# Kernel optimization log

Hardware: AMD Instinct MI355X
Metric: run time of the kernel (lower is better)

The kernel has to match this reference:

```python
import jax, jax.numpy as jnp
import numpy as np

B, N, H = 131072, 64, 8  # batch, n_agents (= n states = n coupling pins, ring), hidden width


def setup_inputs() -> dict:
    key = jax.random.key(0)
    ks = jax.random.split(key, 9)
    x = jax.random.normal(ks[0], (B, N), jnp.float32)
    # per-agent intrinsic MLP (heterogeneous agents, vectorized over agent dim)
    W1 = jax.random.normal(ks[1], (N, H), jnp.float32) * 0.5
    b1 = jax.random.normal(ks[2], (N, H), jnp.float32) * 0.1
    W2 = jax.random.normal(ks[3], (N, H), jnp.float32) * 0.5
    b2 = jax.random.normal(ks[4], (N,), jnp.float32) * 0.1
    # shared coupling MLP: takes [x_send, x_recv] -> scalar contribution
    Wc1 = jax.random.normal(ks[5], (2, H), jnp.float32) * 0.5
    bc1 = jax.random.normal(ks[6], (H,), jnp.float32) * 0.1
    Wc2 = jax.random.normal(ks[7], (H,), jnp.float32) * 0.5
    bc2 = jax.random.normal(ks[8], (1,), jnp.float32) * 0.1
    send_idx = jnp.arange(N, dtype=jnp.int32)
    recv_idx = (send_idx + 1) % N  # ring topology pins (send -> receive), symmetric coupling
    return dict(x=x, W1=W1, b1=b1, W2=W2, b2=b2, Wc1=Wc1, bc1=bc1,
                Wc2=Wc2, bc2=bc2, send_idx=send_idx, recv_idx=recv_idx)


def reference(x, W1, b1, W2, b2, Wc1, bc1, Wc2, bc2, send_idx, recv_idx):
    # ---- coupling_physics: gather pin features, shared MLP, symmetric scatter-add ----
    feats = jnp.stack([x[:, send_idx], x[:, recv_idx]], axis=-1)        # [B, E, 2]
    hc = jnp.tanh(jnp.einsum('bef,fh->beh', feats, Wc1) + bc1)          # [B, E, H]
    contrib = jnp.einsum('beh,h->be', hc, Wc2) + bc2                    # [B, E]
    interactions = (jnp.zeros_like(x)
                    .at[:, recv_idx].add(contrib)    # dx[:, receive] += contribution
                    .at[:, send_idx].add(-contrib))  # dx[:, send]    -= contribution (symmetric)
    # ---- intrinsic_physics: per-agent MLP on own state, plus aggregated interactions ----
    ha = jnp.tanh(x[..., None] * W1 + b1)                               # [B, N, H]
    dx = jnp.einsum('bnh,nh->bn', ha, W2) + b2 + interactions           # [B, N]
    return dx  # [:, :outsize] with outsize == N
```

## Files before the change

kernel.cpp:

```cpp
#include <hip/hip_runtime.h>

static constexpr int N_AGENTS = 64;
static constexpr int H_DIM    = 8;

__device__ __forceinline__ float fast_exp2(float v) {
#if __has_builtin(__builtin_amdgcn_exp2f)
    return __builtin_amdgcn_exp2f(v);
#else
    return exp2f(v);
#endif
}

__device__ __forceinline__ float fast_rcp(float v) {
#if __has_builtin(__builtin_amdgcn_rcpf)
    return __builtin_amdgcn_rcpf(v);
#else
    return 1.0f / v;
#endif
}

__device__ __forceinline__ float fast_tanh(float v) {
    float z = fast_exp2(v * 2.8853900817779268f);
    float r = fast_rcp(z + 1.0f);
    return __builtin_fmaf(-2.0f, r, 1.0f);
}

__global__ __launch_bounds__(256) void networked_ode_kernel(
    const float* __restrict__ x,
    const float* __restrict__ W1,
    const float* __restrict__ b1,
    const float* __restrict__ W2,
    const float* __restrict__ b2,
    const float* __restrict__ Wc1,
    const float* __restrict__ bc1,
    const float* __restrict__ Wc2,
    const float* __restrict__ bc2,
    const int* __restrict__ send_idx,
    const int* __restrict__ recv_idx,
    float* __restrict__ out,
    int B)
{
    const int lane           = threadIdx.x & 63;
    const int wave_in_block  = threadIdx.x >> 6;
    const int waves_per_blk  = blockDim.x >> 6;
    const int gwave          = blockIdx.x * waves_per_blk + wave_in_block;
    const int total_waves    = gridDim.x * waves_per_blk;

    float w1[H_DIM], bb1[H_DIM], w2[H_DIM];
#pragma unroll
    for (int h = 0; h < H_DIM; ++h) {
        w1[h]  = W1[lane * H_DIM + h];
        bb1[h] = b1[lane * H_DIM + h];
        w2[h]  = W2[lane * H_DIM + h];
    }
    const float b2v = b2[lane];

    float wcs[H_DIM], wcr[H_DIM], bc1v[H_DIM], wc2v[H_DIM];
#pragma unroll
    for (int h = 0; h < H_DIM; ++h) {
        wcs[h]  = Wc1[h];
        wcr[h]  = Wc1[H_DIM + h];
        bc1v[h] = bc1[h];
        wc2v[h] = Wc2[h];
    }
    const float bc2v = bc2[0];

    const int sidx = send_idx[lane];
    const int ridx = recv_idx[lane];

    __shared__ int inv_r_s[256], inv_s_s[256];
    const int base = wave_in_block * 64;
    inv_r_s[base + ridx] = lane;
    inv_s_s[base + sidx] = lane;
    __syncthreads();
    const int inv_r = inv_r_s[base + lane];
    const int inv_s = inv_s_s[base + lane];

    for (int row = gwave; row < B; row += total_waves) {
        const float xv = x[(size_t)row * N_AGENTS + lane];
        const float xs = __shfl(xv, sidx, 64);
        const float xr = __shfl(xv, ridx, 64);

        float c = bc2v;
#pragma unroll
        for (int h = 0; h < H_DIM; ++h) {
            float a = __builtin_fmaf(xs, wcs[h], __builtin_fmaf(xr, wcr[h], bc1v[h]));
            c = __builtin_fmaf(fast_tanh(a), wc2v[h], c);
        }

        float acc = b2v;
#pragma unroll
        for (int h = 0; h < H_DIM; ++h) {
            float a = __builtin_fmaf(xv, w1[h], bb1[h]);
            acc = __builtin_fmaf(fast_tanh(a), w2[h], acc);
        }

        const float cr = __shfl(c, inv_r, 64);
        const float cs = __shfl(c, inv_s, 64);

        out[(size_t)row * N_AGENTS + lane] = acc + cr - cs;
    }
}

extern "C" void kernel_launch(void* const* d_in, const int* in_sizes, int n_in,
                              void* d_out, int out_size, void* d_ws, size_t ws_size,
                              hipStream_t stream) {
    const float* x   = (const float*)d_in[0];
    const float* W1  = (const float*)d_in[1];
    const float* b1  = (const float*)d_in[2];
    const float* W2  = (const float*)d_in[3];
    const float* b2  = (const float*)d_in[4];
    const float* Wc1 = (const float*)d_in[5];
    const float* bc1 = (const float*)d_in[6];
    const float* Wc2 = (const float*)d_in[7];
    const float* bc2 = (const float*)d_in[8];
    const int* send_idx = (const int*)d_in[9];
    const int* recv_idx = (const int*)d_in[10];

    const int B = in_sizes[0] / N_AGENTS;

    const int blocks = 2048;
    networked_ode_kernel<<<blocks, dim3(256), 0, stream>>>(
        x, W1, b1, W2, b2, Wc1, bc1, Wc2, bc2, send_idx, recv_idx,
        (float*)d_out, B);
}
```

Before: 130.5 us.

## Use packed fp16 rational tanh and process four rows per wave iteration

Replaces the fp32 exp2/rcp tanh with a clamped Padé rational approximation evaluated in packed half2 arithmetic, where the reciprocal is a bit-trick seed refined by two Newton steps. Each wave now handles four rows per iteration, pairing rows into half2 lanes. It also skips the send shuffle when the send index is the identity. The aim is to cut transcendental and ALU cost per element. In exchange, accumulation and output are done in fp16, which loses precision and may exceed the tolerance.

```diff
diff --git a/kernel.cpp b/kernel.cpp
--- a/kernel.cpp
+++ b/kernel.cpp
@@ -1,28 +1,47 @@
 #include <hip/hip_runtime.h>
+
+typedef _Float16 h2 __attribute__((ext_vector_type(2)));
+typedef unsigned short u2 __attribute__((ext_vector_type(2)));
 
 static constexpr int N_AGENTS = 64;
 static constexpr int H_DIM    = 8;
+static constexpr int ROWS     = 4;
 
-__device__ __forceinline__ float fast_exp2(float v) {
-#if __has_builtin(__builtin_amdgcn_exp2f)
-    return __builtin_amdgcn_exp2f(v);
+__device__ __forceinline__ h2 h2splat(float v) {
+    _Float16 h = (_Float16)v;
+    return (h2){h, h};
+}
+
+__device__ __forceinline__ h2 pack2(float a, float b) {
+#if __has_builtin(__builtin_amdgcn_cvt_pkrtz)
+    auto r = __builtin_amdgcn_cvt_pkrtz(a, b);
+    h2 out; __builtin_memcpy(&out, &r, 4); return out;
 #else
-    return exp2f(v);
+    return (h2){(_Float16)a, (_Float16)b};
 #endif
 }
 
-__device__ __forceinline__ float fast_rcp(float v) {
-#if __has_builtin(__builtin_amdgcn_rcpf)
-    return __builtin_amdgcn_rcpf(v);
-#else
-    return 1.0f / v;
-#endif
-}
+struct TanhConsts {
+    h2 c3p5, mc3p5, c1p, c2p, c1q, c2q, one, two;
+    u2 K;
+};
 
-__device__ __forceinline__ float fast_tanh(float v) {
-    float z = fast_exp2(v * 2.8853900817779268f);
-    float r = fast_rcp(z + 1.0f);
-    return __builtin_fmaf(-2.0f, r, 1.0f);
+__device__ __forceinline__ h2 tanh_pk(h2 t, const TanhConsts& C) {
+    t = __builtin_elementwise_min(t, C.c3p5);
+    t = __builtin_elementwise_max(t, C.mc3p5);
+    const h2 u = t * t;
+    h2 P = __builtin_elementwise_fma(u, C.c2p, C.c1p);
+    P = __builtin_elementwise_fma(u, P, C.one);
+    h2 Q = __builtin_elementwise_fma(u, C.c2q, C.c1q);
+    Q = __builtin_elementwise_fma(u, Q, C.one);
+    u2 qb; __builtin_memcpy(&qb, &Q, 4);
+    u2 rb = C.K - qb;
+    h2 r;  __builtin_memcpy(&r, &rb, 4);
+    h2 m = __builtin_elementwise_fma(-Q, r, C.two);
+    r = r * m;
+    m = __builtin_elementwise_fma(-Q, r, C.two);
+    r = r * m;
+    return (t * P) * r;
 }
 
 __global__ __launch_bounds__(256) void networked_ode_kernel(
@@ -46,27 +65,42 @@
     const int gwave          = blockIdx.x * waves_per_blk + wave_in_block;
     const int total_waves    = gridDim.x * waves_per_blk;
 
-    float w1[H_DIM], bb1[H_DIM], w2[H_DIM];
+    TanhConsts TC;
+    TC.c3p5  = h2splat(3.5f);
+    TC.mc3p5 = h2splat(-3.5f);
+    TC.c1p   = h2splat(105.0f / 945.0f);
+    TC.c2p   = h2splat(1.0f / 945.0f);
+    TC.c1q   = h2splat(420.0f / 945.0f);
+    TC.c2q   = h2splat(15.0f / 945.0f);
+    TC.one   = h2splat(1.0f);
+    TC.two   = h2splat(2.0f);
+    TC.K     = (u2){0x7789, 0x7789};
+
+    float w1v[H_DIM], b1v[H_DIM];
+    h2 w2h[H_DIM];
 #pragma unroll
     for (int h = 0; h < H_DIM; ++h) {
-        w1[h]  = W1[lane * H_DIM + h];
-        bb1[h] = b1[lane * H_DIM + h];
-        w2[h]  = W2[lane * H_DIM + h];
+        w1v[h] = W1[lane * H_DIM + h];
+        b1v[h] = b1[lane * H_DIM + h];
+        w2h[h] = h2splat(W2[lane * H_DIM + h]);
     }
-    const float b2v = b2[lane];
+    const h2 a0h = h2splat(b2[lane]);
 
-    float wcs[H_DIM], wcr[H_DIM], bc1v[H_DIM], wc2v[H_DIM];
+    float wcs[H_DIM], wcr[H_DIM], bc1v[H_DIM];
+    h2 wc2h[H_DIM];
 #pragma unroll
     for (int h = 0; h < H_DIM; ++h) {
         wcs[h]  = Wc1[h];
         wcr[h]  = Wc1[H_DIM + h];
         bc1v[h] = bc1[h];
-        wc2v[h] = Wc2[h];
+        wc2h[h] = h2splat(Wc2[h]);
     }
-    const float bc2v = bc2[0];
+    const h2 c0h = h2splat(bc2[0]);
 
     const int sidx = send_idx[lane];
     const int ridx = recv_idx[lane];
+
+    const bool send_is_id = (__ballot(sidx == lane) == ~0ull);
 
     __shared__ int inv_r_s[256], inv_s_s[256];
     const int base = wave_in_block * 64;
@@ -76,29 +110,61 @@
     const int inv_r = inv_r_s[base + lane];
     const int inv_s = inv_s_s[base + lane];
 
-    for (int row = gwave; row < B; row += total_waves) {
-        const float xv = x[(size_t)row * N_AGENTS + lane];
-        const float xs = __shfl(xv, sidx, 64);
-        const float xr = __shfl(xv, ridx, 64);
-
-        float c = bc2v;
+    for (int row0 = gwave * ROWS; row0 < B; row0 += total_waves * ROWS) {
+        float xv[ROWS], xs[ROWS], xr[ROWS];
 #pragma unroll
-        for (int h = 0; h < H_DIM; ++h) {
-            float a = __builtin_fmaf(xs, wcs[h], __builtin_fmaf(xr, wcr[h], bc1v[h]));
-            c = __builtin_fmaf(fast_tanh(a), wc2v[h], c);
+        for (int k = 0; k < ROWS; ++k) {
+            const int row = row0 + k;
+            xv[k] = (row < B) ? x[(size_t)row * N_AGENTS + lane] : 0.0f;
+        }
+#pragma unroll
+        for (int k = 0; k < ROWS; ++k) xr[k] = __shfl(xv[k], ridx, 64);
+        if (send_is_id) {
+#pragma unroll
+            for (int k = 0; k < ROWS; ++k) xs[k] = xv[k];
+        } else {
+#pragma unroll
+            for (int k = 0; k < ROWS; ++k) xs[k] = __shfl(xv[k], sidx, 64);
         }
 
-        float acc = b2v;
+        h2 C[2] = {c0h, c0h};
+        h2 A[2] = {a0h, a0h};
+
 #pragma unroll
-        for (int h = 0; h < H_DIM; ++h) {
-            float a = __builtin_fmaf(xv, w1[h], bb1[h]);
-            acc = __builtin_fmaf(fast_tanh(a), w2[h], acc);
+        for (int p = 0; p < 2; ++p) {
+            const int r0 = 2 * p, r1 = 2 * p + 1;
+#pragma unroll
+            for (int h = 0; h < H_DIM; ++h) {
+                const float ca0 = __builtin_fmaf(xs[r0], wcs[h],
+                                  __builtin_fmaf(xr[r0], wcr[h], bc1v[h]));
+                const float ca1 = __builtin_fmaf(xs[r1], wcs[h],
+                                  __builtin_fmaf(xr[r1], wcr[h], bc1v[h]));
+                C[p] = __builtin_elementwise_fma(tanh_pk(pack2(ca0, ca1), TC),
+                                                 wc2h[h], C[p]);
+                const float ia0 = __builtin_fmaf(xv[r0], w1v[h], b1v[h]);
+                const float ia1 = __builtin_fmaf(xv[r1], w1v[h], b1v[h]);
+                A[p] = __builtin_elementwise_fma(tanh_pk(pack2(ia0, ia1), TC),
+                                                 w2h[h], A[p]);
+            }
         }
 
-        const float cr = __shfl(c, inv_r, 64);
-        const float cs = __shfl(c, inv_s, 64);
-
-        out[(size_t)row * N_AGENTS + lane] = acc + cr - cs;
+#pragma unroll
+        for (int p = 0; p < 2; ++p) {
+            int cbits; __builtin_memcpy(&cbits, &C[p], 4);
+            const int crb = __shfl(cbits, inv_r, 64);
+            h2 Cr; __builtin_memcpy(&Cr, &crb, 4);
+            h2 Cs;
+            if (send_is_id) {
+                Cs = C[p];
+            } else {
+                const int csb = __shfl(cbits, inv_s, 64);
+                __builtin_memcpy(&Cs, &csb, 4);
+            }
+            const h2 res = A[p] + (Cr - Cs);
+            const int rowa = row0 + 2 * p, rowb = rowa + 1;
+            if (rowa < B) out[(size_t)rowa * N_AGENTS + lane] = (float)res.x;
+            if (rowb < B) out[(size_t)rowb * N_AGENTS + lane] = (float)res.y;
+        }
     }
 }
 
```

Result: no change. 129.8 us (-0.5%).
